# Performance work log

Hardware: AMD Instinct MI355X
Metric: run time of the kernel (lower is better)

## Reference

```python
import jax, jax.numpy as jnp
import numpy as np

N, H = 8192, 256
TOP_K = 16          # k = min(top_k, N-1)
TEMPERATURE = 1.0
NEG_SLOPE = 0.2
NUM_SECTORS = 11


def setup_inputs() -> dict:
    key = jax.random.key(0)
    kE, kW, ka, ks, kA = jax.random.split(key, 5)
    embeddings = jax.random.normal(kE, (N, H), dtype=jnp.float32)
    # xavier-uniform-like scale for W (nn.Linear, bias=False)
    lim = float(np.sqrt(6.0 / (H + H)))
    W = jax.random.uniform(kW, (H, H), dtype=jnp.float32, minval=-lim, maxval=lim)
    # a ~ Normal(0, 1/sqrt(2H))
    a = jax.random.normal(ka, (2 * H,), dtype=jnp.float32) * (1.0 / np.sqrt(2 * H))
    sector_ids = jax.random.randint(ks, (N,), 0, NUM_SECTORS, dtype=jnp.int32)
    active_mask = jax.random.randint(kA, (N,), 0, 2, dtype=jnp.int32).astype(bool)
    return {"embeddings": embeddings, "W": W, "a": a,
            "sector_ids": sector_ids, "active_mask": active_mask}


def reference(embeddings, W, a, sector_ids, active_mask):
    # h = W(embeddings)  (torch Linear: x @ W.T)
    h = embeddings @ W.T                                   # [N, H]
    # attention[i,j] = leaky_relu(a . [h_i, h_j]) = leaky_relu(a1.h_i + a2.h_j)
    # (decomposition of the concat+matmul; same math, avoids O(N^2*2H) tensor)
    a1, a2 = a[:H], a[H:]
    s_i = h @ a1                                           # [N]
    s_j = h @ a2                                           # [N]
    att = jax.nn.leaky_relu(s_i[:, None] + s_j[None, :], NEG_SLOPE) / TEMPERATURE
    # combined mask: active pairs AND same sector
    mask = (active_mask[:, None] & active_mask[None, :]) \
           & (sector_ids[:, None] == sector_ids[None, :])  # [N, N]
    att = jnp.where(mask, att, -jnp.inf)
    k = min(TOP_K, N - 1)
    topk_values, topk_indices = jax.lax.top_k(att, k)      # [N, k] each
    valid = jnp.isfinite(topk_values)                      # invalid = masked-out slots
    # dense padded representation of (edge_index, edge_weight):
    # src = topk_indices, dst = row index, weight = topk_values where valid
    edge_weight = jnp.where(valid, topk_values, 0.0)
    return edge_weight, topk_indices, valid
```

## Files before the change

kernel.cpp:

```cpp
#include <hip/hip_runtime.h>

#define N 8192
#define H 256
#define TOPK 16
#define NSEC 11
#define NEG_SLOPE 0.2
#define NB 256
#define NT 256
#define RPB (N / NB)
#define NSL 8
#define SLICE (N / NSL)
#define IDX_SENT 0x7fffffff

__device__ __forceinline__ bool better(double av, int ai, double bv, int bi) {
    return (av > bv) || (av == bv && ai < bi);
}

__global__ __launch_bounds__(NT) void compute_v_s(
    const float* __restrict__ E, const float* __restrict__ W,
    const float* __restrict__ a,
    float* __restrict__ s1f, double* __restrict__ s2g,
    int* __restrict__ arrive)
{
    __shared__ float sa[2 * H];
    __shared__ double sv1[H];
    __shared__ double sv2[H];

    int t = threadIdx.x;
    int blk = blockIdx.x;
    int lane = t & 63;
    int w = t >> 6;

    if (blk == 0 && t < NSEC) arrive[t] = 0;

    sa[t] = a[t];
    sa[t + H] = a[t + H];
    __syncthreads();

    {
        double a1_0 = 0.0, a1_1 = 0.0, a1_2 = 0.0, a1_3 = 0.0;
        double a2_0 = 0.0, a2_1 = 0.0, a2_2 = 0.0, a2_3 = 0.0;
        for (int j = 0; j < H; j += 4) {
            double w0 = (double)W[(j + 0) * H + t];
            double w1 = (double)W[(j + 1) * H + t];
            double w2 = (double)W[(j + 2) * H + t];
            double w3 = (double)W[(j + 3) * H + t];
            a1_0 += w0 * (double)sa[j + 0];
            a1_1 += w1 * (double)sa[j + 1];
            a1_2 += w2 * (double)sa[j + 2];
            a1_3 += w3 * (double)sa[j + 3];
            a2_0 += w0 * (double)sa[H + j + 0];
            a2_1 += w1 * (double)sa[H + j + 1];
            a2_2 += w2 * (double)sa[H + j + 2];
            a2_3 += w3 * (double)sa[H + j + 3];
        }
        sv1[t] = (a1_0 + a1_1) + (a1_2 + a1_3);
        sv2[t] = (a2_0 + a2_1) + (a2_2 + a2_3);
    }
    __syncthreads();

    {
        float4 e[RPB / 4];
#pragma unroll
        for (int q = 0; q < RPB / 4; ++q) {
            int row = blk * RPB + (w + 4 * q);
            e[q] = ((const float4*)(E + (size_t)row * H))[lane];
        }
        int base = lane * 4;
        double b10 = sv1[base + 0], b11 = sv1[base + 1],
               b12 = sv1[base + 2], b13 = sv1[base + 3];
        double b20 = sv2[base + 0], b21 = sv2[base + 1],
               b22 = sv2[base + 2], b23 = sv2[base + 3];
#pragma unroll
        for (int q = 0; q < RPB / 4; ++q) {
            int row = blk * RPB + (w + 4 * q);
            double acc1 = (double)e[q].x * b10 + (double)e[q].y * b11 +
                          (double)e[q].z * b12 + (double)e[q].w * b13;
            double acc2 = (double)e[q].x * b20 + (double)e[q].y * b21 +
                          (double)e[q].z * b22 + (double)e[q].w * b23;
            for (int o = 32; o > 0; o >>= 1) {
                acc1 += __shfl_down(acc1, o);
                acc2 += __shfl_down(acc2, o);
            }
            if (lane == 0) {
                s1f[row] = (float)acc1;
                s2g[row] = acc2;
            }
        }
    }
}

__global__ __launch_bounds__(NT) void slice_merge(
    const double* __restrict__ s2g, const int* __restrict__ sec,
    const int* __restrict__ act,
    double* __restrict__ candV, int* __restrict__ candI,
    int* __restrict__ cnts, int* __restrict__ arrive,
    int* __restrict__ top_idx, int* __restrict__ fill_idx,
    int* __restrict__ m_arr)
{
    __shared__ double wV[4][TOPK];
    __shared__ int wI[4][TOPK];
    __shared__ int wCnt[4];
    __shared__ int sLast;

    int bx = blockIdx.x;
    int c = bx >> 3;
    int sl = bx & 7;
    int t = threadIdx.x;
    int lane = t & 63;
    int w = t >> 6;

    int j0 = sl * SLICE + 4 * t;
    int4 a4 = *(const int4*)(act + j0);
    int4 s4 = *(const int4*)(sec + j0);
    double2 d01 = *(const double2*)(s2g + j0);
    double2 d23 = *(const double2*)(s2g + j0 + 2);

    bool p0 = (a4.x != 0) && (s4.x == c);
    bool p1 = (a4.y != 0) && (s4.y == c);
    bool p2 = (a4.z != 0) && (s4.z == c);
    bool p3 = (a4.w != 0) && (s4.w == c);

    double v[4];
    int ix[4];
    v[0] = p0 ? d01.x : -INFINITY;  ix[0] = p0 ? (j0 + 0) : IDX_SENT;
    v[1] = p1 ? d01.y : -INFINITY;  ix[1] = p1 ? (j0 + 1) : IDX_SENT;
    v[2] = p2 ? d23.x : -INFINITY;  ix[2] = p2 ? (j0 + 2) : IDX_SENT;
    v[3] = p3 ? d23.y : -INFINITY;  ix[3] = p3 ? (j0 + 3) : IDX_SENT;

    int cnt = __popcll(__ballot(p0)) + __popcll(__ballot(p1)) +
              __popcll(__ballot(p2)) + __popcll(__ballot(p3));

    for (int r = 0; r < TOPK; ++r) {
        double bv = v[0];
        int bi = ix[0];
#pragma unroll
        for (int p = 1; p < 4; ++p)
            if (better(v[p], ix[p], bv, bi)) { bv = v[p]; bi = ix[p]; }
        for (int o = 32; o > 0; o >>= 1) {
            double ov = __shfl_xor(bv, o);
            int oi = __shfl_xor(bi, o);
            if (better(ov, oi, bv, bi)) { bv = ov; bi = oi; }
        }
#pragma unroll
        for (int p = 0; p < 4; ++p)
            if (ix[p] == bi) { v[p] = -INFINITY; ix[p] = IDX_SENT; }
        if (lane == 0) {
            wV[w][r] = bv;
            wI[w][r] = bi;
        }
    }
    if (lane == 0) wCnt[w] = cnt;
    __syncthreads();

    if (w == 0) {
        double mv = wV[lane >> 4][lane & 15];
        int mi = wI[lane >> 4][lane & 15];
        for (int r = 0; r < TOPK; ++r) {
            double bv = mv;
            int bi = mi;
            for (int o = 32; o > 0; o >>= 1) {
                double ov = __shfl_xor(bv, o);
                int oi = __shfl_xor(bi, o);
                if (better(ov, oi, bv, bi)) { bv = ov; bi = oi; }
            }
            if (mi == bi) { mv = -INFINITY; mi = IDX_SENT; }
            if (lane == 0) {
                candV[bx * TOPK + r] = bv;
                candI[bx * TOPK + r] = bi;
            }
        }
        if (lane == 0) {
            cnts[bx] = wCnt[0] + wCnt[1] + wCnt[2] + wCnt[3];
            __threadfence();
            int old = atomicAdd(&arrive[c], 1);
            sLast = (old == NSL - 1);
        }
    }
    __syncthreads();
    if (!sLast) return;

    __threadfence();

    if (w == 0) {
        const double* cbV = candV + (size_t)c * NSL * TOPK;
        const int* cbI = candI + (size_t)c * NSL * TOPK;
        double v0 = cbV[lane];
        int i0 = cbI[lane];
        double v1 = cbV[lane + 64];
        int i1 = cbI[lane + 64];
        for (int r = 0; r < TOPK; ++r) {
            double bv;
            int bi;
            if (better(v0, i0, v1, i1)) { bv = v0; bi = i0; }
            else                        { bv = v1; bi = i1; }
            for (int o = 32; o > 0; o >>= 1) {
                double ov = __shfl_xor(bv, o);
                int oi = __shfl_xor(bi, o);
                if (better(ov, oi, bv, bi)) { bv = ov; bi = oi; }
            }
            if (i0 == bi)      { v0 = -INFINITY; i0 = IDX_SENT; }
            else if (i1 == bi) { v1 = -INFINITY; i1 = IDX_SENT; }
            if (lane == 0) top_idx[c * TOPK + r] = (bi == IDX_SENT) ? -1 : bi;
        }
        int cl = (lane < NSL) ? cnts[c * NSL + lane] : 0;
        for (int o = 32; o > 0; o >>= 1) cl += __shfl_xor(cl, o);
        if (lane == 0) m_arr[c] = (cl < TOPK) ? cl : TOPK;
    } else if (w == 1) {
        int cnt2 = 0;
        for (int basej = 0; basej < N && cnt2 < TOPK; basej += 64) {
            int j = basej + lane;
            bool fail = !((act[j] != 0) && (sec[j] == c));
            unsigned long long mask = __ballot(fail);
            if (fail) {
                int rank = cnt2 + __popcll(mask & ((1ull << lane) - 1));
                if (rank < TOPK) fill_idx[c * TOPK + rank] = j;
            }
            cnt2 += __popcll(mask);
        }
    }
}

__global__ __launch_bounds__(NT) void write_out(const float* __restrict__ s1f,
                                                const double* __restrict__ s2g,
                                                const int* __restrict__ sec,
                                                const int* __restrict__ act,
                                                const int* __restrict__ top_idx,
                                                const int* __restrict__ fill_idx,
                                                const int* __restrict__ m_arr,
                                                float* __restrict__ out) {
    int gid = blockIdx.x * NT + threadIdx.x;
    int i = gid >> 4;
    int slot = gid & 15;

    float wgt = 0.0f;
    float fidx;
    float fvalid = 0.0f;

    if (act[i] == 0) {
        fidx = (float)slot;
    } else {
        int c = sec[i];
        int m = m_arr[c];
        if (slot < m) {
            int j = top_idx[c * TOPK + slot];
            double x = (double)s1f[i] + s2g[j];
            double attv = (x >= 0.0) ? x : NEG_SLOPE * x;
            wgt = (float)attv;
            fvalid = 1.0f;
            fidx = (float)j;
        } else {
            fidx = (float)fill_idx[c * TOPK + (slot - m)];
        }
    }

    out[gid] = wgt;
    out[N * TOPK + gid] = fidx;
    out[2 * N * TOPK + gid] = fvalid;
}

extern "C" void kernel_launch(void* const* d_in, const int* in_sizes, int n_in,
                              void* d_out, int out_size, void* d_ws, size_t ws_size,
                              hipStream_t stream) {
    const float* E = (const float*)d_in[0];
    const float* W = (const float*)d_in[1];
    const float* a = (const float*)d_in[2];
    const int* sec = (const int*)d_in[3];
    const int* act = (const int*)d_in[4];

    char* ws = (char*)d_ws;
    double* s2g = (double*)ws;
    double* candV = s2g + N;
    float* s1f = (float*)(candV + NSEC * NSL * TOPK);
    int* candI = (int*)(s1f + N);
    int* cnts = candI + NSEC * NSL * TOPK;
    int* top_idx = cnts + NSEC * NSL;
    int* fill_idx = top_idx + NSEC * TOPK;
    int* m_arr = fill_idx + NSEC * TOPK;
    int* arrive = m_arr + NSEC;

    float* out = (float*)d_out;

    hipLaunchKernelGGL(compute_v_s, dim3(NB), dim3(NT), 0, stream,
                       E, W, a, s1f, s2g, arrive);
    hipLaunchKernelGGL(slice_merge, dim3(NSEC * NSL), dim3(NT), 0, stream,
                       s2g, sec, act, candV, candI, cnts, arrive,
                       top_idx, fill_idx, m_arr);
    hipLaunchKernelGGL(write_out, dim3((N * TOPK) / NT), dim3(NT), 0, stream,
                       s1f, s2g, sec, act, top_idx, fill_idx, m_arr, out);
}
```

Before: 113.4 us.

## Fuse three kernels into one cooperative kernel with grid-wide syncs

```diff
diff --git a/kernel.cpp b/kernel.cpp
--- a/kernel.cpp
+++ b/kernel.cpp
@@ -1,4 +1,7 @@
 #include <hip/hip_runtime.h>
+#include <hip/hip_cooperative_groups.h>
+
+namespace cg = cooperative_groups;
 
 #define N 8192
 #define H 256
@@ -16,22 +19,32 @@
     return (av > bv) || (av == bv && ai < bi);
 }
 
-__global__ __launch_bounds__(NT) void compute_v_s(
+__global__ __launch_bounds__(NT) void fused_all(
     const float* __restrict__ E, const float* __restrict__ W,
-    const float* __restrict__ a,
+    const float* __restrict__ a, const int* __restrict__ sec,
+    const int* __restrict__ act,
     float* __restrict__ s1f, double* __restrict__ s2g,
-    int* __restrict__ arrive)
+    double* __restrict__ candV, int* __restrict__ candI,
+    int* __restrict__ cnts, int* __restrict__ arrive,
+    int* __restrict__ top_idx, int* __restrict__ fill_idx,
+    int* __restrict__ m_arr, float* __restrict__ out)
 {
+    cg::grid_group grid = cg::this_grid();
+
     __shared__ float sa[2 * H];
     __shared__ double sv1[H];
     __shared__ double sv2[H];
+    __shared__ double wV[4][TOPK];
+    __shared__ int wI[4][TOPK];
+    __shared__ int wCnt[4];
+    __shared__ int sLast;
 
     int t = threadIdx.x;
-    int blk = blockIdx.x;
+    int bx = blockIdx.x;
     int lane = t & 63;
     int w = t >> 6;
 
-    if (blk == 0 && t < NSEC) arrive[t] = 0;
+    if (bx == 0 && t < NSEC) arrive[t] = 0;
 
     sa[t] = a[t];
     sa[t + H] = a[t + H];
@@ -63,7 +76,7 @@
         float4 e[RPB / 4];
 #pragma unroll
         for (int q = 0; q < RPB / 4; ++q) {
-            int row = blk * RPB + (w + 4 * q);
+            int row = bx * RPB + (w + 4 * q);
             e[q] = ((const float4*)(E + (size_t)row * H))[lane];
         }
         int base = lane * 4;
@@ -73,7 +86,7 @@
                b22 = sv2[base + 2], b23 = sv2[base + 3];
 #pragma unroll
         for (int q = 0; q < RPB / 4; ++q) {
-            int row = blk * RPB + (w + 4 * q);
+            int row = bx * RPB + (w + 4 * q);
             double acc1 = (double)e[q].x * b10 + (double)e[q].y * b11 +
                           (double)e[q].z * b12 + (double)e[q].w * b13;
             double acc2 = (double)e[q].x * b20 + (double)e[q].y * b21 +
@@ -88,175 +101,158 @@
             }
         }
     }
-}
-
-__global__ __launch_bounds__(NT) void slice_merge(
-    const double* __restrict__ s2g, const int* __restrict__ sec,
-    const int* __restrict__ act,
-    double* __restrict__ candV, int* __restrict__ candI,
-    int* __restrict__ cnts, int* __restrict__ arrive,
-    int* __restrict__ top_idx, int* __restrict__ fill_idx,
-    int* __restrict__ m_arr)
-{
-    __shared__ double wV[4][TOPK];
-    __shared__ int wI[4][TOPK];
-    __shared__ int wCnt[4];
-    __shared__ int sLast;
-
-    int bx = blockIdx.x;
-    int c = bx >> 3;
-    int sl = bx & 7;
-    int t = threadIdx.x;
-    int lane = t & 63;
-    int w = t >> 6;
-
-    int j0 = sl * SLICE + 4 * t;
-    int4 a4 = *(const int4*)(act + j0);
-    int4 s4 = *(const int4*)(sec + j0);
-    double2 d01 = *(const double2*)(s2g + j0);
-    double2 d23 = *(const double2*)(s2g + j0 + 2);
-
-    bool p0 = (a4.x != 0) && (s4.x == c);
-    bool p1 = (a4.y != 0) && (s4.y == c);
-    bool p2 = (a4.z != 0) && (s4.z == c);
-    bool p3 = (a4.w != 0) && (s4.w == c);
-
-    double v[4];
-    int ix[4];
-    v[0] = p0 ? d01.x : -INFINITY;  ix[0] = p0 ? (j0 + 0) : IDX_SENT;
-    v[1] = p1 ? d01.y : -INFINITY;  ix[1] = p1 ? (j0 + 1) : IDX_SENT;
-    v[2] = p2 ? d23.x : -INFINITY;  ix[2] = p2 ? (j0 + 2) : IDX_SENT;
-    v[3] = p3 ? d23.y : -INFINITY;  ix[3] = p3 ? (j0 + 3) : IDX_SENT;
-
-    int cnt = __popcll(__ballot(p0)) + __popcll(__ballot(p1)) +
-              __popcll(__ballot(p2)) + __popcll(__ballot(p3));
-
-    for (int r = 0; r < TOPK; ++r) {
-        double bv = v[0];
-        int bi = ix[0];
-#pragma unroll
-        for (int p = 1; p < 4; ++p)
-            if (better(v[p], ix[p], bv, bi)) { bv = v[p]; bi = ix[p]; }
-        for (int o = 32; o > 0; o >>= 1) {
-            double ov = __shfl_xor(bv, o);
-            int oi = __shfl_xor(bi, o);
-            if (better(ov, oi, bv, bi)) { bv = ov; bi = oi; }
-        }
-#pragma unroll
-        for (int p = 0; p < 4; ++p)
-            if (ix[p] == bi) { v[p] = -INFINITY; ix[p] = IDX_SENT; }
-        if (lane == 0) {
-            wV[w][r] = bv;
-            wI[w][r] = bi;
-        }
-    }
-    if (lane == 0) wCnt[w] = cnt;
-    __syncthreads();
-
-    if (w == 0) {
-        double mv = wV[lane >> 4][lane & 15];
-        int mi = wI[lane >> 4][lane & 15];
+
+    __threadfence();
+    grid.sync();
+
+    if (bx < NSEC * NSL) {
+        int c = bx >> 3;
+        int sl = bx & 7;
+
+        int j0 = sl * SLICE + 4 * t;
+        int4 a4 = *(const int4*)(act + j0);
+        int4 s4 = *(const int4*)(sec + j0);
+        double2 d01 = *(const double2*)(s2g + j0);
+        double2 d23 = *(const double2*)(s2g + j0 + 2);
+
+        bool p0 = (a4.x != 0) && (s4.x == c);
+        bool p1 = (a4.y != 0) && (s4.y == c);
+        bool p2 = (a4.z != 0) && (s4.z == c);
+        bool p3 = (a4.w != 0) && (s4.w == c);
+
+        double v[4];
+        int ix[4];
+        v[0] = p0 ? d01.x : -INFINITY;  ix[0] = p0 ? (j0 + 0) : IDX_SENT;
+        v[1] = p1 ? d01.y : -INFINITY;  ix[1] = p1 ? (j0 + 1) : IDX_SENT;
+        v[2] = p2 ? d23.x : -INFINITY;  ix[2] = p2 ? (j0 + 2) : IDX_SENT;
+        v[3] = p3 ? d23.y : -INFINITY;  ix[3] = p3 ? (j0 + 3) : IDX_SENT;
+
+        int cnt = __popcll(__ballot(p0)) + __popcll(__ballot(p1)) +
+                  __popcll(__ballot(p2)) + __popcll(__ballot(p3));
+
         for (int r = 0; r < TOPK; ++r) {
-            double bv = mv;
-            int bi = mi;
+            double bv = v[0];
+            int bi = ix[0];
+#pragma unroll
+            for (int p = 1; p < 4; ++p)
+                if (better(v[p], ix[p], bv, bi)) { bv = v[p]; bi = ix[p]; }
             for (int o = 32; o > 0; o >>= 1) {
                 double ov = __shfl_xor(bv, o);
                 int oi = __shfl_xor(bi, o);
                 if (better(ov, oi, bv, bi)) { bv = ov; bi = oi; }
             }
-            if (mi == bi) { mv = -INFINITY; mi = IDX_SENT; }
+#pragma unroll
+            for (int p = 0; p < 4; ++p)
+                if (ix[p] == bi) { v[p] = -INFINITY; ix[p] = IDX_SENT; }
             if (lane == 0) {
-                candV[bx * TOPK + r] = bv;
-                candI[bx * TOPK + r] = bi;
-            }
-        }
-        if (lane == 0) {
-            cnts[bx] = wCnt[0] + wCnt[1] + wCnt[2] + wCnt[3];
+                wV[w][r] = bv;
+                wI[w][r] = bi;
+            }
+        }
+        if (lane == 0) wCnt[w] = cnt;
+        __syncthreads();
+
+        if (w == 0) {
+            double mv = wV[lane >> 4][lane & 15];
+            int mi = wI[lane >> 4][lane & 15];
+            for (int r = 0; r < TOPK; ++r) {
+                double bv = mv;
+                int bi = mi;
+                for (int o = 32; o > 0; o >>= 1) {
+                    double ov = __shfl_xor(bv, o);
+                    int oi = __shfl_xor(bi, o);
+                    if (better(ov, oi, bv, bi)) { bv = ov; bi = oi; }
+                }
+                if (mi == bi) { mv = -INFINITY; mi = IDX_SENT; }
+                if (lane == 0) {
+                    candV[bx * TOPK + r] = bv;
+                    candI[bx * TOPK + r] = bi;
+                }
+            }
+            if (lane == 0) {
+                cnts[bx] = wCnt[0] + wCnt[1] + wCnt[2] + wCnt[3];
+                __threadfence();
+                int old = atomicAdd(&arrive[c], 1);
+                sLast = (old == NSL - 1);
+            }
+        }
+        __syncthreads();
+
+        if (sLast) {
             __threadfence();
-            int old = atomicAdd(&arrive[c], 1);
-            sLast = (old == NSL - 1);
-        }
-    }
-    __syncthreads();
-    if (!sLast) return;
+
+            if (w == 0) {
+                const double* cbV = candV + (size_t)c * NSL * TOPK;
+                const int* cbI = candI + (size_t)c * NSL * TOPK;
+                double v0 = cbV[lane];
+                int i0 = cbI[lane];
+                double v1 = cbV[lane + 64];
+                int i1 = cbI[lane + 64];
+                for (int r = 0; r < TOPK; ++r) {
+                    double bv;
+                    int bi;
+                    if (better(v0, i0, v1, i1)) { bv = v0; bi = i0; }
+                    else                        { bv = v1; bi = i1; }
+                    for (int o = 32; o > 0; o >>= 1) {
+                        double ov = __shfl_xor(bv, o);
+                        int oi = __shfl_xor(bi, o);
+                        if (better(ov, oi, bv, bi)) { bv = ov; bi = oi; }
+                    }
+                    if (i0 == bi)      { v0 = -INFINITY; i0 = IDX_SENT; }
+                    else if (i1 == bi) { v1 = -INFINITY; i1 = IDX_SENT; }
+                    if (lane == 0) top_idx[c * TOPK + r] = (bi == IDX_SENT) ? -1 : bi;
+                }
+                int cl = (lane < NSL) ? cnts[c * NSL + lane] : 0;
+                for (int o = 32; o > 0; o >>= 1) cl += __shfl_xor(cl, o);
+                if (lane == 0) m_arr[c] = (cl < TOPK) ? cl : TOPK;
+            } else if (w == 1) {
+                int cnt2 = 0;
+                for (int basej = 0; basej < N && cnt2 < TOPK; basej += 64) {
+                    int j = basej + lane;
+                    bool fail = !((act[j] != 0) && (sec[j] == c));
+                    unsigned long long mask = __ballot(fail);
+                    if (fail) {
+                        int rank = cnt2 + __popcll(mask & ((1ull << lane) - 1));
+                        if (rank < TOPK) fill_idx[c * TOPK + rank] = j;
+                    }
+                    cnt2 += __popcll(mask);
+                }
+            }
+        }
+    }
 
     __threadfence();
-
-    if (w == 0) {
-        const double* cbV = candV + (size_t)c * NSL * TOPK;
-        const int* cbI = candI + (size_t)c * NSL * TOPK;
-        double v0 = cbV[lane];
-        int i0 = cbI[lane];
-        double v1 = cbV[lane + 64];
-        int i1 = cbI[lane + 64];
-        for (int r = 0; r < TOPK; ++r) {
-            double bv;
-            int bi;
-            if (better(v0, i0, v1, i1)) { bv = v0; bi = i0; }
-            else                        { bv = v1; bi = i1; }
-            for (int o = 32; o > 0; o >>= 1) {
-                double ov = __shfl_xor(bv, o);
-                int oi = __shfl_xor(bi, o);
-                if (better(ov, oi, bv, bi)) { bv = ov; bi = oi; }
-            }
-            if (i0 == bi)      { v0 = -INFINITY; i0 = IDX_SENT; }
-            else if (i1 == bi) { v1 = -INFINITY; i1 = IDX_SENT; }
-            if (lane == 0) top_idx[c * TOPK + r] = (bi == IDX_SENT) ? -1 : bi;
-        }
-        int cl = (lane < NSL) ? cnts[c * NSL + lane] : 0;
-        for (int o = 32; o > 0; o >>= 1) cl += __shfl_xor(cl, o);
-        if (lane == 0) m_arr[c] = (cl < TOPK) ? cl : TOPK;
-    } else if (w == 1) {
-        int cnt2 = 0;
-        for (int basej = 0; basej < N && cnt2 < TOPK; basej += 64) {
-            int j = basej + lane;
-            bool fail = !((act[j] != 0) && (sec[j] == c));
-            unsigned long long mask = __ballot(fail);
-            if (fail) {
-                int rank = cnt2 + __popcll(mask & ((1ull << lane) - 1));
-                if (rank < TOPK) fill_idx[c * TOPK + rank] = j;
-            }
-            cnt2 += __popcll(mask);
-        }
-    }
-}
-
-__global__ __launch_bounds__(NT) void write_out(const float* __restrict__ s1f,
-                                                const double* __restrict__ s2g,
-                                                const int* __restrict__ sec,
-                                                const int* __restrict__ act,
-                                                const int* __restrict__ top_idx,
-                                                const int* __restrict__ fill_idx,
-                                                const int* __restrict__ m_arr,
-                                                float* __restrict__ out) {
-    int gid = blockIdx.x * NT + threadIdx.x;
-    int i = gid >> 4;
-    int slot = gid & 15;
-
-    float wgt = 0.0f;
-    float fidx;
-    float fvalid = 0.0f;
-
-    if (act[i] == 0) {
-        fidx = (float)slot;
-    } else {
-        int c = sec[i];
-        int m = m_arr[c];
-        if (slot < m) {
-            int j = top_idx[c * TOPK + slot];
-            double x = (double)s1f[i] + s2g[j];
-            double attv = (x >= 0.0) ? x : NEG_SLOPE * x;
-            wgt = (float)attv;
-            fvalid = 1.0f;
-            fidx = (float)j;
+    grid.sync();
+
+    for (int gid = bx * NT + t; gid < N * TOPK; gid += NB * NT) {
+        int i = gid >> 4;
+        int slot = gid & 15;
+
+        float wgt = 0.0f;
+        float fidx;
+        float fvalid = 0.0f;
+
+        if (act[i] == 0) {
+            fidx = (float)slot;
         } else {
-            fidx = (float)fill_idx[c * TOPK + (slot - m)];
-        }
-    }
-
-    out[gid] = wgt;
-    out[N * TOPK + gid] = fidx;
-    out[2 * N * TOPK + gid] = fvalid;
+            int c = sec[i];
+            int m = m_arr[c];
+            if (slot < m) {
+                int j = top_idx[c * TOPK + slot];
+                double x = (double)s1f[i] + s2g[j];
+                double attv = (x >= 0.0) ? x : NEG_SLOPE * x;
+                wgt = (float)attv;
+                fvalid = 1.0f;
+                fidx = (float)j;
+            } else {
+                fidx = (float)fill_idx[c * TOPK + (slot - m)];
+            }
+        }
+
+        out[gid] = wgt;
+        out[N * TOPK + gid] = fidx;
+        out[2 * N * TOPK + gid] = fvalid;
+    }
 }
 
 extern "C" void kernel_launch(void* const* d_in, const int* in_sizes, int n_in,
@@ -281,11 +277,12 @@
 
     float* out = (float*)d_out;
 
-    hipLaunchKernelGGL(compute_v_s, dim3(NB), dim3(NT), 0, stream,
-                       E, W, a, s1f, s2g, arrive);
-    hipLaunchKernelGGL(slice_merge, dim3(NSEC * NSL), dim3(NT), 0, stream,
-                       s2g, sec, act, candV, candI, cnts, arrive,
-                       top_idx, fill_idx, m_arr);
-    hipLaunchKernelGGL(write_out, dim3((N * TOPK) / NT), dim3(NT), 0, stream,
-                       s1f, s2g, sec, act, top_idx, fill_idx, m_arr, out);
+    void* args[] = {
+        (void*)&E, (void*)&W, (void*)&a, (void*)&sec, (void*)&act,
+        (void*)&s1f, (void*)&s2g, (void*)&candV, (void*)&candI,
+        (void*)&cnts, (void*)&arrive, (void*)&top_idx, (void*)&fill_idx,
+        (void*)&m_arr, (void*)&out
+    };
+    hipLaunchCooperativeKernel((const void*)fused_all, dim3(NB), dim3(NT),
+                               args, 0, stream);
 }
```

Result: slower. 188.0 us (+65.8%).

## Fuse slice-merge top-k and output write into one kernel with grid barrier

Applied to the files above, without the earlier changes.

```diff
diff --git a/kernel.cpp b/kernel.cpp
--- a/kernel.cpp
+++ b/kernel.cpp
@@ -10,6 +10,7 @@
 #define RPB (N / NB)
 #define NSL 8
 #define SLICE (N / NSL)
+#define NWB 256
 #define IDX_SENT 0x7fffffff
 
 __device__ __forceinline__ bool better(double av, int ai, double bv, int bi) {
@@ -31,7 +32,7 @@
     int lane = t & 63;
     int w = t >> 6;
 
-    if (blk == 0 && t < NSEC) arrive[t] = 0;
+    if (blk == 0 && t <= NSEC) arrive[t] = 0;
 
     sa[t] = a[t];
     sa[t + H] = a[t + H];
@@ -90,13 +91,13 @@
     }
 }
 
-__global__ __launch_bounds__(NT) void slice_merge(
-    const double* __restrict__ s2g, const int* __restrict__ sec,
-    const int* __restrict__ act,
+__global__ __launch_bounds__(NT) void slice_merge_write(
+    const float* __restrict__ s1f, const double* __restrict__ s2g,
+    const int* __restrict__ sec, const int* __restrict__ act,
     double* __restrict__ candV, int* __restrict__ candI,
     int* __restrict__ cnts, int* __restrict__ arrive,
     int* __restrict__ top_idx, int* __restrict__ fill_idx,
-    int* __restrict__ m_arr)
+    int* __restrict__ m_arr, float* __restrict__ out)
 {
     __shared__ double wV[4][TOPK];
     __shared__ int wI[4][TOPK];
@@ -104,159 +105,170 @@
     __shared__ int sLast;
 
     int bx = blockIdx.x;
-    int c = bx >> 3;
-    int sl = bx & 7;
     int t = threadIdx.x;
     int lane = t & 63;
     int w = t >> 6;
-
-    int j0 = sl * SLICE + 4 * t;
-    int4 a4 = *(const int4*)(act + j0);
-    int4 s4 = *(const int4*)(sec + j0);
-    double2 d01 = *(const double2*)(s2g + j0);
-    double2 d23 = *(const double2*)(s2g + j0 + 2);
-
-    bool p0 = (a4.x != 0) && (s4.x == c);
-    bool p1 = (a4.y != 0) && (s4.y == c);
-    bool p2 = (a4.z != 0) && (s4.z == c);
-    bool p3 = (a4.w != 0) && (s4.w == c);
-
-    double v[4];
-    int ix[4];
-    v[0] = p0 ? d01.x : -INFINITY;  ix[0] = p0 ? (j0 + 0) : IDX_SENT;
-    v[1] = p1 ? d01.y : -INFINITY;  ix[1] = p1 ? (j0 + 1) : IDX_SENT;
-    v[2] = p2 ? d23.x : -INFINITY;  ix[2] = p2 ? (j0 + 2) : IDX_SENT;
-    v[3] = p3 ? d23.y : -INFINITY;  ix[3] = p3 ? (j0 + 3) : IDX_SENT;
-
-    int cnt = __popcll(__ballot(p0)) + __popcll(__ballot(p1)) +
-              __popcll(__ballot(p2)) + __popcll(__ballot(p3));
-
-    for (int r = 0; r < TOPK; ++r) {
-        double bv = v[0];
-        int bi = ix[0];
+    int* done = arrive + NSEC;
+
+    if (bx < NSEC * NSL) {
+        int c = bx >> 3;
+        int sl = bx & 7;
+
+        int j0 = sl * SLICE + 4 * t;
+        int4 a4 = *(const int4*)(act + j0);
+        int4 s4 = *(const int4*)(sec + j0);
+        double2 d01 = *(const double2*)(s2g + j0);
+        double2 d23 = *(const double2*)(s2g + j0 + 2);
+
+        bool p0 = (a4.x != 0) && (s4.x == c);
+        bool p1 = (a4.y != 0) && (s4.y == c);
+        bool p2 = (a4.z != 0) && (s4.z == c);
+        bool p3 = (a4.w != 0) && (s4.w == c);
+
+        double v[4];
+        int ix[4];
+        v[0] = p0 ? d01.x : -INFINITY;  ix[0] = p0 ? (j0 + 0) : IDX_SENT;
+        v[1] = p1 ? d01.y : -INFINITY;  ix[1] = p1 ? (j0 + 1) : IDX_SENT;
+        v[2] = p2 ? d23.x : -INFINITY;  ix[2] = p2 ? (j0 + 2) : IDX_SENT;
+        v[3] = p3 ? d23.y : -INFINITY;  ix[3] = p3 ? (j0 + 3) : IDX_SENT;
+
+        int cnt = __popcll(__ballot(p0)) + __popcll(__ballot(p1)) +
+                  __popcll(__ballot(p2)) + __popcll(__ballot(p3));
+
+        for (int r = 0; r < TOPK; ++r) {
+            double bv = v[0];
+            int bi = ix[0];
 #pragma unroll
-        for (int p = 1; p < 4; ++p)
-            if (better(v[p], ix[p], bv, bi)) { bv = v[p]; bi = ix[p]; }
-        for (int o = 32; o > 0; o >>= 1) {
-            double ov = __shfl_xor(bv, o);
-            int oi = __shfl_xor(bi, o);
-            if (better(ov, oi, bv, bi)) { bv = ov; bi = oi; }
-        }
-#pragma unroll
-        for (int p = 0; p < 4; ++p)
-            if (ix[p] == bi) { v[p] = -INFINITY; ix[p] = IDX_SENT; }
-        if (lane == 0) {
-            wV[w][r] = bv;
-            wI[w][r] = bi;
-        }
-    }
-    if (lane == 0) wCnt[w] = cnt;
-    __syncthreads();
-
-    if (w == 0) {
-        double mv = wV[lane >> 4][lane & 15];
-        int mi = wI[lane >> 4][lane & 15];
-        for (int r = 0; r < TOPK; ++r) {
-            double bv = mv;
-            int bi = mi;
+            for (int p = 1; p < 4; ++p)
+                if (better(v[p], ix[p], bv, bi)) { bv = v[p]; bi = ix[p]; }
             for (int o = 32; o > 0; o >>= 1) {
                 double ov = __shfl_xor(bv, o);
                 int oi = __shfl_xor(bi, o);
                 if (better(ov, oi, bv, bi)) { bv = ov; bi = oi; }
             }
-            if (mi == bi) { mv = -INFINITY; mi = IDX_SENT; }
+#pragma unroll
+            for (int p = 0; p < 4; ++p)
+                if (ix[p] == bi) { v[p] = -INFINITY; ix[p] = IDX_SENT; }
             if (lane == 0) {
-                candV[bx * TOPK + r] = bv;
-                candI[bx * TOPK + r] = bi;
-            }
-        }
-        if (lane == 0) {
-            cnts[bx] = wCnt[0] + wCnt[1] + wCnt[2] + wCnt[3];
+                wV[w][r] = bv;
+                wI[w][r] = bi;
+            }
+        }
+        if (lane == 0) wCnt[w] = cnt;
+        __syncthreads();
+
+        if (w == 0) {
+            double mv = wV[lane >> 4][lane & 15];
+            int mi = wI[lane >> 4][lane & 15];
+            for (int r = 0; r < TOPK; ++r) {
+                double bv = mv;
+                int bi = mi;
+                for (int o = 32; o > 0; o >>= 1) {
+                    double ov = __shfl_xor(bv, o);
+                    int oi = __shfl_xor(bi, o);
+                    if (better(ov, oi, bv, bi)) { bv = ov; bi = oi; }
+                }
+                if (mi == bi) { mv = -INFINITY; mi = IDX_SENT; }
+                if (lane == 0) {
+                    candV[bx * TOPK + r] = bv;
+                    candI[bx * TOPK + r] = bi;
+                }
+            }
+            if (lane == 0) {
+                cnts[bx] = wCnt[0] + wCnt[1] + wCnt[2] + wCnt[3];
+                __threadfence();
+                int old = atomicAdd(&arrive[c], 1);
+                sLast = (old == NSL - 1);
+            }
+        }
+        __syncthreads();
+
+        if (sLast) {
             __threadfence();
-            int old = atomicAdd(&arrive[c], 1);
-            sLast = (old == NSL - 1);
+
+            if (w == 0) {
+                const double* cbV = candV + (size_t)c * NSL * TOPK;
+                const int* cbI = candI + (size_t)c * NSL * TOPK;
+                double v0 = cbV[lane];
+                int i0 = cbI[lane];
+                double v1 = cbV[lane + 64];
+                int i1 = cbI[lane + 64];
+                for (int r = 0; r < TOPK; ++r) {
+                    double bv;
+                    int bi;
+                    if (better(v0, i0, v1, i1)) { bv = v0; bi = i0; }
+                    else                        { bv = v1; bi = i1; }
+                    for (int o = 32; o > 0; o >>= 1) {
+                        double ov = __shfl_xor(bv, o);
+                        int oi = __shfl_xor(bi, o);
+                        if (better(ov, oi, bv, bi)) { bv = ov; bi = oi; }
+                    }
+                    if (i0 == bi)      { v0 = -INFINITY; i0 = IDX_SENT; }
+                    else if (i1 == bi) { v1 = -INFINITY; i1 = IDX_SENT; }
+                    if (lane == 0) top_idx[c * TOPK + r] = (bi == IDX_SENT) ? -1 : bi;
+                }
+                int cl = (lane < NSL) ? cnts[c * NSL + lane] : 0;
+                for (int o = 32; o > 0; o >>= 1) cl += __shfl_xor(cl, o);
+                if (lane == 0) m_arr[c] = (cl < TOPK) ? cl : TOPK;
+            } else if (w == 1) {
+                int cnt2 = 0;
+                for (int basej = 0; basej < N && cnt2 < TOPK; basej += 64) {
+                    int j = basej + lane;
+                    bool fail = !((act[j] != 0) && (sec[j] == c));
+                    unsigned long long mask = __ballot(fail);
+                    if (fail) {
+                        int rank = cnt2 + __popcll(mask & ((1ull << lane) - 1));
+                        if (rank < TOPK) fill_idx[c * TOPK + rank] = j;
+                    }
+                    cnt2 += __popcll(mask);
+                }
+            }
+            __syncthreads();
+            if (t == 0) {
+                __threadfence();
+                atomicAdd(done, 1);
+            }
+        }
+    }
+
+    if (t == 0) {
+        while (__hip_atomic_load(done, __ATOMIC_RELAXED,
+                                 __HIP_MEMORY_SCOPE_AGENT) < NSEC) {
+            __builtin_amdgcn_s_sleep(8);
         }
     }
     __syncthreads();
-    if (!sLast) return;
-
     __threadfence();
 
-    if (w == 0) {
-        const double* cbV = candV + (size_t)c * NSL * TOPK;
-        const int* cbI = candI + (size_t)c * NSL * TOPK;
-        double v0 = cbV[lane];
-        int i0 = cbI[lane];
-        double v1 = cbV[lane + 64];
-        int i1 = cbI[lane + 64];
-        for (int r = 0; r < TOPK; ++r) {
-            double bv;
-            int bi;
-            if (better(v0, i0, v1, i1)) { bv = v0; bi = i0; }
-            else                        { bv = v1; bi = i1; }
-            for (int o = 32; o > 0; o >>= 1) {
-                double ov = __shfl_xor(bv, o);
-                int oi = __shfl_xor(bi, o);
-                if (better(ov, oi, bv, bi)) { bv = ov; bi = oi; }
-            }
-            if (i0 == bi)      { v0 = -INFINITY; i0 = IDX_SENT; }
-            else if (i1 == bi) { v1 = -INFINITY; i1 = IDX_SENT; }
-            if (lane == 0) top_idx[c * TOPK + r] = (bi == IDX_SENT) ? -1 : bi;
-        }
-        int cl = (lane < NSL) ? cnts[c * NSL + lane] : 0;
-        for (int o = 32; o > 0; o >>= 1) cl += __shfl_xor(cl, o);
-        if (lane == 0) m_arr[c] = (cl < TOPK) ? cl : TOPK;
-    } else if (w == 1) {
-        int cnt2 = 0;
-        for (int basej = 0; basej < N && cnt2 < TOPK; basej += 64) {
-            int j = basej + lane;
-            bool fail = !((act[j] != 0) && (sec[j] == c));
-            unsigned long long mask = __ballot(fail);
-            if (fail) {
-                int rank = cnt2 + __popcll(mask & ((1ull << lane) - 1));
-                if (rank < TOPK) fill_idx[c * TOPK + rank] = j;
-            }
-            cnt2 += __popcll(mask);
-        }
-    }
-}
-
-__global__ __launch_bounds__(NT) void write_out(const float* __restrict__ s1f,
-                                                const double* __restrict__ s2g,
-                                                const int* __restrict__ sec,
-                                                const int* __restrict__ act,
-                                                const int* __restrict__ top_idx,
-                                                const int* __restrict__ fill_idx,
-                                                const int* __restrict__ m_arr,
-                                                float* __restrict__ out) {
-    int gid = blockIdx.x * NT + threadIdx.x;
-    int i = gid >> 4;
-    int slot = gid & 15;
-
-    float wgt = 0.0f;
-    float fidx;
-    float fvalid = 0.0f;
-
-    if (act[i] == 0) {
-        fidx = (float)slot;
-    } else {
-        int c = sec[i];
-        int m = m_arr[c];
-        if (slot < m) {
-            int j = top_idx[c * TOPK + slot];
-            double x = (double)s1f[i] + s2g[j];
-            double attv = (x >= 0.0) ? x : NEG_SLOPE * x;
-            wgt = (float)attv;
-            fvalid = 1.0f;
-            fidx = (float)j;
+    for (int gid = bx * NT + t; gid < N * TOPK; gid += NWB * NT) {
+        int i = gid >> 4;
+        int slot = gid & 15;
+
+        float wgt = 0.0f;
+        float fidx;
+        float fvalid = 0.0f;
+
+        if (act[i] == 0) {
+            fidx = (float)slot;
         } else {
-            fidx = (float)fill_idx[c * TOPK + (slot - m)];
-        }
-    }
-
-    out[gid] = wgt;
-    out[N * TOPK + gid] = fidx;
-    out[2 * N * TOPK + gid] = fvalid;
+            int c = sec[i];
+            int m = m_arr[c];
+            if (slot < m) {
+                int j = top_idx[c * TOPK + slot];
+                double x = (double)s1f[i] + s2g[j];
+                double attv = (x >= 0.0) ? x : NEG_SLOPE * x;
+                wgt = (float)attv;
+                fvalid = 1.0f;
+                fidx = (float)j;
+            } else {
+                fidx = (float)fill_idx[c * TOPK + (slot - m)];
+            }
+        }
+
+        out[gid] = wgt;
+        out[N * TOPK + gid] = fidx;
+        out[2 * N * TOPK + gid] = fvalid;
+    }
 }
 
 extern "C" void kernel_launch(void* const* d_in, const int* in_sizes, int n_in,
@@ -283,9 +295,7 @@
 
     hipLaunchKernelGGL(compute_v_s, dim3(NB), dim3(NT), 0, stream,
                        E, W, a, s1f, s2g, arrive);
-    hipLaunchKernelGGL(slice_merge, dim3(NSEC * NSL), dim3(NT), 0, stream,
-                       s2g, sec, act, candV, candI, cnts, arrive,
-                       top_idx, fill_idx, m_arr);
-    hipLaunchKernelGGL(write_out, dim3((N * TOPK) / NT), dim3(NT), 0, stream,
-                       s1f, s2g, sec, act, top_idx, fill_idx, m_arr, out);
+    hipLaunchKernelGGL(slice_merge_write, dim3(NWB), dim3(NT), 0, stream,
+                       s1f, s2g, sec, act, candV, candI, cnts, arrive,
+                       top_idx, fill_idx, m_arr, out);
 }
```

Result: slower. 132.6 us (+16.9%).
